# Kernel tuning notes

Hardware: AMD Instinct MI355X
Metric: run time of the kernel (lower is better)

The kernel has to match this reference:

```python
import jax, jax.numpy as jnp
import numpy as np

B, N, P, T = 128, 64, 128, 168


def setup_inputs() -> dict:
    key = jax.random.key(0)
    k1, k2, k3, k4, k5 = jax.random.split(key, 5)
    x = jax.random.normal(k1, (B, N, P), dtype=jnp.float32)
    x_i = jax.random.randint(k2, (B, P), 0, T)
    g = jax.random.normal(k3, (N * N, N * N), dtype=jnp.float32)
    weights = jax.random.normal(k4, (N * N, 1), dtype=jnp.float32)
    alphas = jax.random.uniform(k5, (1, T), dtype=jnp.float32)
    return {"x": x, "x_i": x_i, "g": g, "weights": weights, "alphas": alphas}


def reference(x, x_i, g, weights, alphas):
    # x: [b, N, p], x_i: [b, p] int in [0, T), g: [N*N, N*N]
    n = x.shape[1]
    F = (g @ (weights ** 2)) @ alphas          # [N*N, T]
    wg = F.T.reshape(-1, n, n)                 # [T, N, N]
    f_ = wg[x_i]                               # [b, p, N, N] (gather)
    xt = jnp.swapaxes(x, 1, 2)                 # [b, p, N]
    # matmul(f_, x_[...,None]) then sum over (p, last) == einsum then sum over p
    Z = jnp.einsum('bpij,bpj->bi', f_, xt)     # [b, N]
    return (Z, F)
```

## Files before the change

kernel.cpp:

```cpp
#include <hip/hip_runtime.h>


#define GN 4096
#define TT 168
#define BB 128
#define NN 64
#define PP 128

__global__ __launch_bounds__(256) void k_fused(
    const float* __restrict__ x, const int* __restrict__ xi,
    const float* __restrict__ g, const float* __restrict__ w,
    const float* __restrict__ alphas, float* __restrict__ v,
    float* __restrict__ y, float* __restrict__ Fout) {
  const int t = threadIdx.x;
  if (blockIdx.x >= BB) {
    const int rb = blockIdx.x - BB;
    const int wave = t >> 6, lane = t & 63;
    const int row = rb * 4 + wave;
    const float4* g4 = (const float4*)(g + (size_t)row * GN);
    const float4* w4 = (const float4*)w;
    float s = 0.f;
#pragma unroll 8
    for (int it = 0; it < 16; ++it) {
      float4 a = g4[it * 64 + lane];
      float4 b = w4[it * 64 + lane];
      s += a.x * (b.x * b.x) + a.y * (b.y * b.y) +
           a.z * (b.z * b.z) + a.w * (b.w * b.w);
    }
#pragma unroll
    for (int off = 32; off; off >>= 1) s += __shfl_xor(s, off, 64);
    if (lane == 0) v[row] = s;
    float* Frow = Fout + (size_t)row * TT;
    Frow[lane]      = s * alphas[lane];
    Frow[64 + lane] = s * alphas[64 + lane];
    if (lane < TT - 128) Frow[128 + lane] = s * alphas[128 + lane];
  } else {
    const int b = blockIdx.x;
    __shared__ float ap[PP];
    if (t < PP) ap[t] = alphas[xi[b * PP + t]];
    __syncthreads();
    const int j = t >> 2, r = t & 3;
    const float4* xrow4 =
        (const float4*)(x + (size_t)b * (NN * PP) + (size_t)j * PP + r * 32);
    const float4* ap4 = (const float4*)(ap + r * 32);
    float s = 0.f;
#pragma unroll
    for (int k = 0; k < 8; ++k) {
      float4 a = xrow4[k];
      float4 c = ap4[k];
      s += a.x * c.x + a.y * c.y + a.z * c.z + a.w * c.w;
    }
    s += __shfl_down(s, 2, 64);
    s += __shfl_down(s, 1, 64);
    if (r == 0) y[b * NN + j] = s;
  }
}

__global__ __launch_bounds__(64) void k_z2(
    const float* __restrict__ v, const float* __restrict__ y,
    float* __restrict__ Z) {
  const int b = blockIdx.x, i = threadIdx.x;
  const float4* v4 = (const float4*)(v + i * NN);
  const float4* y4 = (const float4*)(y + b * NN);
  float z = 0.f;
#pragma unroll
  for (int q = 0; q < 16; ++q) {
    float4 a = v4[q];
    float4 c = y4[q];
    z += a.x * c.x + a.y * c.y + a.z * c.z + a.w * c.w;
  }
  Z[b * NN + i] = z;
}

extern "C" void kernel_launch(void* const* d_in, const int* in_sizes, int n_in,
                              void* d_out, int out_size, void* d_ws, size_t ws_size,
                              hipStream_t stream) {
  const float* x      = (const float*)d_in[0];
  const int*   xi     = (const int*)  d_in[1];
  const float* g      = (const float*)d_in[2];
  const float* w      = (const float*)d_in[3];
  const float* alphas = (const float*)d_in[4];

  float* Z    = (float*)d_out;
  float* Fout = (float*)d_out + (BB * NN);
  float* v    = (float*)d_ws;
  float* y    = (float*)d_ws + GN;

  k_fused<<<BB + GN / 4, 256, 0, stream>>>(x, xi, g, w, alphas, v, y, Fout);
  k_z2<<<BB, 64, 0, stream>>>(v, y, Z);
}
```

Baseline: 104.3 us.

## Fuse Z reduction into main kernel using atomic counter grid sync

Merges the second kernel into the first. Row-reduction blocks increment a global atomic counter when they finish, and the batch blocks spin on that counter before computing Z from v and a shared-memory y. Row blocks are reordered to come first so they get scheduled before the spinning blocks, which avoids deadlock. This removes one kernel launch and the y round-trip through global memory. It adds a memset, a spin-wait, and a reliance on block scheduling order for forward progress.

```diff
diff --git a/kernel.cpp b/kernel.cpp
--- a/kernel.cpp
+++ b/kernel.cpp
@@ -6,17 +6,18 @@
 #define BB 128
 #define NN 64
 #define PP 128
+#define NROWBLK 1024
 
-__global__ __launch_bounds__(256) void k_fused(
+__global__ __launch_bounds__(256) void k_all(
     const float* __restrict__ x, const int* __restrict__ xi,
     const float* __restrict__ g, const float* __restrict__ w,
     const float* __restrict__ alphas, float* __restrict__ v,
-    float* __restrict__ y, float* __restrict__ Fout) {
+    unsigned int* __restrict__ cnt, float* __restrict__ Z,
+    float* __restrict__ Fout) {
   const int t = threadIdx.x;
-  if (blockIdx.x >= BB) {
-    const int rb = blockIdx.x - BB;
+  if (blockIdx.x < NROWBLK) {
     const int wave = t >> 6, lane = t & 63;
-    const int row = rb * 4 + wave;
+    const int row = blockIdx.x * 4 + wave;
     const float4* g4 = (const float4*)(g + (size_t)row * GN);
     const float4* w4 = (const float4*)w;
     float s = 0.f;
@@ -34,9 +35,16 @@
     Frow[lane]      = s * alphas[lane];
     Frow[64 + lane] = s * alphas[64 + lane];
     if (lane < TT - 128) Frow[128 + lane] = s * alphas[128 + lane];
+    __syncthreads();
+    if (t == 0) {
+      __threadfence();
+      __hip_atomic_fetch_add(cnt, 1u, __ATOMIC_RELEASE,
+                             __HIP_MEMORY_SCOPE_AGENT);
+    }
   } else {
-    const int b = blockIdx.x;
+    const int b = blockIdx.x - NROWBLK;
     __shared__ float ap[PP];
+    __shared__ float ysh[NN];
     if (t < PP) ap[t] = alphas[xi[b * PP + t]];
     __syncthreads();
     const int j = t >> 2, r = t & 3;
@@ -52,24 +60,29 @@
     }
     s += __shfl_down(s, 2, 64);
     s += __shfl_down(s, 1, 64);
-    if (r == 0) y[b * NN + j] = s;
+    if (r == 0) ysh[j] = s;
+    if (t == 0) {
+      while (__hip_atomic_load(cnt, __ATOMIC_ACQUIRE,
+                               __HIP_MEMORY_SCOPE_AGENT) < NROWBLK) {
+        __builtin_amdgcn_s_sleep(8);
+      }
+      __threadfence();
+    }
+    __syncthreads();
+    const int i = t >> 2;
+    const float4* v4 = (const float4*)(v + i * NN + r * 16);
+    const float4* y4 = (const float4*)(ysh + r * 16);
+    float z = 0.f;
+#pragma unroll
+    for (int q = 0; q < 4; ++q) {
+      float4 a = v4[q];
+      float4 c = y4[q];
+      z += a.x * c.x + a.y * c.y + a.z * c.z + a.w * c.w;
+    }
+    z += __shfl_down(z, 2, 64);
+    z += __shfl_down(z, 1, 64);
+    if (r == 0) Z[b * NN + i] = z;
   }
-}
-
-__global__ __launch_bounds__(64) void k_z2(
-    const float* __restrict__ v, const float* __restrict__ y,
-    float* __restrict__ Z) {
-  const int b = blockIdx.x, i = threadIdx.x;
-  const float4* v4 = (const float4*)(v + i * NN);
-  const float4* y4 = (const float4*)(y + b * NN);
-  float z = 0.f;
-#pragma unroll
-  for (int q = 0; q < 16; ++q) {
-    float4 a = v4[q];
-    float4 c = y4[q];
-    z += a.x * c.x + a.y * c.y + a.z * c.z + a.w * c.w;
-  }
-  Z[b * NN + i] = z;
 }
 
 extern "C" void kernel_launch(void* const* d_in, const int* in_sizes, int n_in,
@@ -84,8 +97,8 @@
   float* Z    = (float*)d_out;
   float* Fout = (float*)d_out + (BB * NN);
   float* v    = (float*)d_ws;
-  float* y    = (float*)d_ws + GN;
+  unsigned int* cnt = (unsigned int*)((float*)d_ws + GN);
 
-  k_fused<<<BB + GN / 4, 256, 0, stream>>>(x, xi, g, w, alphas, v, y, Fout);
-  k_z2<<<BB, 64, 0, stream>>>(v, y, Z);
+  hipMemsetAsync(cnt, 0, sizeof(unsigned int), stream);
+  k_all<<<NROWBLK + BB, 256, 0, stream>>>(x, xi, g, w, alphas, v, cnt, Z, Fout);
 }
```

New measurement: 189.5 us. 81.7% more time.
